# Optimization experiments

Measured on AMD Instinct MI355X. Metric: run time of the kernel, lower is better.

The kernel has to match this reference:

```python
import jax, jax.numpy as jnp
import numpy as np

D_MODEL, N_HEADS, D_K, D_V = 1024, 16, 64, 64
B, S = 4, 1024
LN_EPS = 1e-5


def setup_inputs() -> dict:
    key = jax.random.key(0)
    ks = jax.random.split(key, 12)
    s = 0.02
    # causal mask: True = masked (mimics masked_fill_ semantics)
    mask = jnp.triu(jnp.ones((S, S), dtype=bool), k=1)
    mask = jnp.broadcast_to(mask, (B, S, S))
    return {
        "Q": jax.random.normal(ks[0], (B, S, D_MODEL), jnp.float32),
        "K": jax.random.normal(ks[1], (B, S, D_MODEL), jnp.float32),
        "V": jax.random.normal(ks[2], (B, S, D_MODEL), jnp.float32),
        "mask": mask,
        # Linear params stored as [in, out] (equivalent to torch weight.T)
        "Wq": jax.random.normal(ks[3], (D_MODEL, N_HEADS * D_K), jnp.float32) * s,
        "bq": jnp.zeros((N_HEADS * D_K,), jnp.float32),
        "Wk": jax.random.normal(ks[4], (D_MODEL, N_HEADS * D_K), jnp.float32) * s,
        "bk": jnp.zeros((N_HEADS * D_K,), jnp.float32),
        "Wv": jax.random.normal(ks[5], (D_MODEL, N_HEADS * D_V), jnp.float32) * s,
        "bv": jnp.zeros((N_HEADS * D_V,), jnp.float32),
        "Wo": jax.random.normal(ks[6], (N_HEADS * D_V, D_MODEL), jnp.float32) * s,
        "bo": jnp.zeros((D_MODEL,), jnp.float32),
        "gamma": jnp.ones((D_MODEL,), jnp.float32),
        "beta": jnp.zeros((D_MODEL,), jnp.float32),
    }


def reference(Q, K, V, mask, Wq, bq, Wk, bk, Wv, bv, Wo, bo, gamma, beta):
    b, sq, _ = Q.shape
    sk = K.shape[1]
    residual = Q
    # projections -> [b, h, s, d]
    q = (Q @ Wq + bq).reshape(b, sq, N_HEADS, D_K).transpose(0, 2, 1, 3)
    k = (K @ Wk + bk).reshape(b, sk, N_HEADS, D_K).transpose(0, 2, 1, 3)
    v = (V @ Wv + bv).reshape(b, sk, N_HEADS, D_V).transpose(0, 2, 1, 3)
    scale = 1.0 / np.sqrt(D_K).astype(np.float32)
    scores = jnp.einsum("bhqd,bhkd->bhqk", q, k) * scale  # [b,h,sq,sk]
    scores = jnp.where(mask[:, None, :, :], jnp.float32(-1e9), scores)
    attn = jax.nn.softmax(scores, axis=-1)
    out = jnp.einsum("bhqk,bhkd->bhqd", attn, v)
    out = out.transpose(0, 2, 1, 3).reshape(b, sq, N_HEADS * D_V)
    out = out @ Wo + bo
    # LayerNorm(out + residual)
    x = out + residual
    mu = jnp.mean(x, axis=-1, keepdims=True)
    var = jnp.mean(jnp.square(x - mu), axis=-1, keepdims=True)
    y = (x - mu) * jax.lax.rsqrt(var + LN_EPS) * gamma + beta
    return (y, attn)
```

## Files before the change

kernel.cpp:

```cpp
#include <hip/hip_runtime.h>
#include <stdint.h>

#define B_ 4
#define S_ 1024
#define H_ 16
#define D_ 64
#define DM 1024
#define M_ (B_*S_)

using bf16x8 = __attribute__((ext_vector_type(8))) short;
using f32x4  = __attribute__((ext_vector_type(4))) float;

__device__ inline unsigned short f2bf(float f) {
  unsigned u = __float_as_uint(f);
  u += 0x7fff + ((u >> 16) & 1);
  return (unsigned short)(u >> 16);
}
__device__ inline float bf2f(unsigned short s) {
  return __uint_as_float(((unsigned)s) << 16);
}

__global__ __launch_bounds__(256) void cvt_f32_bf16(const float* __restrict__ src,
                                                    unsigned short* __restrict__ dst, int n4) {
  int i = blockIdx.x * 256 + threadIdx.x;
  if (i < n4) {
    float4 v = ((const float4*)src)[i];
    ushort4 o;
    o.x = f2bf(v.x); o.y = f2bf(v.y); o.z = f2bf(v.z); o.w = f2bf(v.w);
    ((ushort4*)dst)[i] = o;
  }
}

__global__ __launch_bounds__(256) void transpose_cvt(const float* w0, const float* w1,
                                                     const float* w2, const float* w3,
                                                     unsigned short* o0, unsigned short* o1,
                                                     unsigned short* o2, unsigned short* o3) {
  const float* src; unsigned short* dst;
  switch (blockIdx.z) {
    case 0: src = w0; dst = o0; break;
    case 1: src = w1; dst = o1; break;
    case 2: src = w2; dst = o2; break;
    default: src = w3; dst = o3; break;
  }
  __shared__ float t[32][33];
  int tx = threadIdx.x, ty = threadIdx.y;
  int x = blockIdx.x * 32 + tx;
  for (int i = 0; i < 4; i++) {
    int y = blockIdx.y * 32 + ty + i * 8;
    t[ty + i * 8][tx] = src[y * DM + x];
  }
  __syncthreads();
  int xo = blockIdx.y * 32 + tx;
  for (int i = 0; i < 4; i++) {
    int yo = blockIdx.x * 32 + ty + i * 8;
    dst[yo * DM + xo] = f2bf(t[tx][ty + i * 8]);
  }
}

__global__ __launch_bounds__(256) void gemm_nt(const unsigned short* __restrict__ X,
                                               const unsigned short* __restrict__ WT,
                                               const float* __restrict__ bias,
                                               void* __restrict__ out, int mode) {
  __shared__ unsigned short Al[64][32];
  __shared__ unsigned short Bl[64][32];
  int t = threadIdx.x;
  int lane = t & 63, w = t >> 6;
  int quad = lane >> 4, l16 = lane & 15;
  int wm = w & 1, wn = w >> 1;
  int m0 = blockIdx.y * 64, n0 = blockIdx.x * 64;
  f32x4 acc[2][2] = {};
  int arow = t >> 2, acol = (t & 3) * 8;
  for (int k0 = 0; k0 < DM; k0 += 32) {
    *(uint4*)&Al[arow][acol] = *(const uint4*)&X [((size_t)(m0 + arow)) * DM + k0 + acol];
    *(uint4*)&Bl[arow][acol] = *(const uint4*)&WT[((size_t)(n0 + arow)) * DM + k0 + acol];
    __syncthreads();
    bf16x8 af[2], bf[2];
    for (int ms = 0; ms < 2; ms++) af[ms] = *(const bf16x8*)&Al[wm * 32 + ms * 16 + l16][quad * 8];
    for (int ns = 0; ns < 2; ns++) bf[ns] = *(const bf16x8*)&Bl[wn * 32 + ns * 16 + l16][quad * 8];
    for (int ms = 0; ms < 2; ms++)
      for (int ns = 0; ns < 2; ns++)
        acc[ms][ns] = __builtin_amdgcn_mfma_f32_16x16x32_bf16(af[ms], bf[ns], acc[ms][ns], 0, 0, 0);
    __syncthreads();
  }
  for (int ms = 0; ms < 2; ms++)
    for (int ns = 0; ns < 2; ns++)
      for (int r = 0; r < 4; r++) {
        int gm = m0 + wm * 32 + ms * 16 + quad * 4 + r;
        int gn = n0 + wn * 32 + ns * 16 + l16;
        float v = acc[ms][ns][r] + bias[gn];
        if (mode == 2) {
          ((float*)out)[(size_t)gm * DM + gn] = v;
        } else {
          int b = gm >> 10, s = gm & 1023, h = gn >> 6, d = gn & 63;
          if (mode == 0)
            ((unsigned short*)out)[(((size_t)(b * H_ + h)) * S_ + s) * D_ + d] = f2bf(v);
          else
            ((unsigned short*)out)[(((size_t)(b * H_ + h)) * D_ + d) * S_ + s] = f2bf(v);
        }
      }
}

__global__ __launch_bounds__(256) void attn_kernel(const unsigned short* __restrict__ qp,
                                                   const unsigned short* __restrict__ kp,
                                                   const unsigned short* __restrict__ vT,
                                                   float* __restrict__ attn_out,
                                                   unsigned short* __restrict__ ctx) {
  __shared__ unsigned short Srow[16][1032];
  __shared__ unsigned short Qt[16][64];
  __shared__ float red[16][16];
  __shared__ float rmax[16];
  __shared__ float rinv[16];
  int t = threadIdx.x;
  int lane = t & 63, w = t >> 6, quad = lane >> 4, l16 = lane & 15;
  int bx = blockIdx.x;
  int qt = bx & 63, h = (bx >> 6) & 15, b = bx >> 10;
  int bh = b * H_ + h;
  const int L = (qt + 1) * 16;

  {
    int r = t >> 4, d = (t & 15) * 4;
    const unsigned short* src = qp + (((size_t)bh * S_) + qt * 16 + r) * D_ + d;
    ushort4 v = *(const ushort4*)src;
    Qt[r][d + 0] = f2bf(bf2f(v.x) * 0.125f);
    Qt[r][d + 1] = f2bf(bf2f(v.y) * 0.125f);
    Qt[r][d + 2] = f2bf(bf2f(v.z) * 0.125f);
    Qt[r][d + 3] = f2bf(bf2f(v.w) * 0.125f);
  }
  __syncthreads();

  for (int ct = w; ct <= qt; ct += 4) {
    f32x4 acc = {};
    for (int d0 = 0; d0 < 64; d0 += 32) {
      bf16x8 af = *(const bf16x8*)&Qt[l16][d0 + quad * 8];
      bf16x8 bfr = *(const bf16x8*)&kp[(((size_t)bh * S_) + ct * 16 + l16) * D_ + d0 + quad * 8];
      acc = __builtin_amdgcn_mfma_f32_16x16x32_bf16(af, bfr, acc, 0, 0, 0);
    }
    for (int r = 0; r < 4; r++) {
      int row = quad * 4 + r;
      int gq = qt * 16 + row, gk = ct * 16 + l16;
      Srow[row][ct * 16 + l16] = f2bf((gk <= gq) ? acc[r] : -1e30f);
    }
  }
  __syncthreads();

  int row = t & 15, chunk = t >> 4;
  float m = -1e30f;
  for (int c = chunk; c < L; c += 16) m = fmaxf(m, bf2f(Srow[row][c]));
  red[row][chunk] = m;
  __syncthreads();
  if (t < 16) {
    float mm = -1e30f;
    for (int j = 0; j < 16; j++) mm = fmaxf(mm, red[t][j]);
    rmax[t] = mm;
  }
  __syncthreads();
  float mr = rmax[row], sum = 0.f;
  for (int c = chunk; c < L; c += 16) {
    float e = __expf(bf2f(Srow[row][c]) - mr);
    Srow[row][c] = f2bf(e);
    sum += e;
  }
  red[row][chunk] = sum;
  __syncthreads();
  if (t < 16) {
    float l = 0.f;
    for (int j = 0; j < 16; j++) l += red[t][j];
    rinv[t] = 1.0f / l;
  }
  __syncthreads();

  float* outbase = attn_out + (((size_t)bh) * S_ + qt * 16) * S_;
  for (int idx = t; idx < 16 * 1024; idx += 256) {
    int rr = idx >> 10, cc = idx & 1023;
    float v = (cc < L) ? bf2f(Srow[rr][cc]) * rinv[rr] : 0.f;
    outbase[(size_t)rr * S_ + cc] = v;
  }
  if (L & 31) {
    Srow[t & 15][L + (t >> 4)] = 0;
  }
  __syncthreads();

  int K32 = (L + 31) >> 5;
  f32x4 oacc = {};
  int n = w * 16 + l16;
  for (int kk = 0; kk < K32; kk++) {
    int k0 = kk * 32;
    bf16x8 af = *(const bf16x8*)&Srow[l16][k0 + quad * 8];
    bf16x8 bfr = *(const bf16x8*)&vT[(((size_t)bh) * D_ + n) * S_ + k0 + quad * 8];
    oacc = __builtin_amdgcn_mfma_f32_16x16x32_bf16(af, bfr, oacc, 0, 0, 0);
  }
  for (int r = 0; r < 4; r++) {
    int rr = quad * 4 + r;
    ctx[(((size_t)b * S_) + qt * 16 + rr) * DM + h * D_ + n] = f2bf(oacc[r] * rinv[rr]);
  }
}

__global__ __launch_bounds__(256) void ln_kernel(const float* __restrict__ y0,
                                                 const float* __restrict__ resid,
                                                 const float* __restrict__ gamma,
                                                 const float* __restrict__ beta,
                                                 float* __restrict__ out) {
  int row = blockIdx.x, t = threadIdx.x;
  float x[4]; float s = 0.f, s2 = 0.f;
  for (int i = 0; i < 4; i++) {
    int c = t + i * 256;
    float v = y0[(size_t)row * DM + c] + resid[(size_t)row * DM + c];
    x[i] = v; s += v; s2 += v * v;
  }
  for (int off = 32; off; off >>= 1) {
    s  += __shfl_down(s,  off, 64);
    s2 += __shfl_down(s2, off, 64);
  }
  __shared__ float ws1[4], ws2[4];
  __shared__ float mu_s, rv_s;
  int wv = t >> 6, lane = t & 63;
  if (lane == 0) { ws1[wv] = s; ws2[wv] = s2; }
  __syncthreads();
  if (t == 0) {
    float ts = ws1[0] + ws1[1] + ws1[2] + ws1[3];
    float ts2 = ws2[0] + ws2[1] + ws2[2] + ws2[3];
    float mu = ts / DM;
    float var = ts2 / DM - mu * mu;
    mu_s = mu; rv_s = rsqrtf(var + 1e-5f);
  }
  __syncthreads();
  float mu = mu_s, rv = rv_s;
  for (int i = 0; i < 4; i++) {
    int c = t + i * 256;
    out[(size_t)row * DM + c] = (x[i] - mu) * rv * gamma[c] + beta[c];
  }
}

extern "C" void kernel_launch(void* const* d_in, const int* in_sizes, int n_in,
                              void* d_out, int out_size, void* d_ws, size_t ws_size,
                              hipStream_t stream) {
  const float* Qf = (const float*)d_in[0];
  const float* Kf = (const float*)d_in[1];
  const float* Vf = (const float*)d_in[2];
  const float* Wq = (const float*)d_in[4];
  const float* bq = (const float*)d_in[5];
  const float* Wk = (const float*)d_in[6];
  const float* bk = (const float*)d_in[7];
  const float* Wv = (const float*)d_in[8];
  const float* bv = (const float*)d_in[9];
  const float* Wo = (const float*)d_in[10];
  const float* bo = (const float*)d_in[11];
  const float* gamma = (const float*)d_in[12];
  const float* beta  = (const float*)d_in[13];

  char* ws = (char*)d_ws;
  unsigned short* Qb  = (unsigned short*)(ws + 0);
  unsigned short* ctx = (unsigned short*)(ws + 0);
  unsigned short* Kb  = (unsigned short*)(ws + 8388608);
  unsigned short* Vb  = (unsigned short*)(ws + 16777216);
  float*          y0  = (float*)(ws + 8388608);
  unsigned short* WqT = (unsigned short*)(ws + 25165824);
  unsigned short* WkT = (unsigned short*)(ws + 27262976);
  unsigned short* WvT = (unsigned short*)(ws + 29360128);
  unsigned short* WoT = (unsigned short*)(ws + 31457280);
  unsigned short* qp  = (unsigned short*)(ws + 33554432);
  unsigned short* kp  = (unsigned short*)(ws + 41943040);
  unsigned short* vTp = (unsigned short*)(ws + 50331648);

  float* y_out    = (float*)d_out;
  float* attn_out = (float*)d_out + (size_t)M_ * DM;

  int n4 = M_ * DM / 4;
  cvt_f32_bf16<<<dim3(n4 / 256), dim3(256), 0, stream>>>(Qf, Qb, n4);
  cvt_f32_bf16<<<dim3(n4 / 256), dim3(256), 0, stream>>>(Kf, Kb, n4);
  cvt_f32_bf16<<<dim3(n4 / 256), dim3(256), 0, stream>>>(Vf, Vb, n4);
  transpose_cvt<<<dim3(32, 32, 4), dim3(32, 8), 0, stream>>>(Wq, Wk, Wv, Wo, WqT, WkT, WvT, WoT);

  dim3 ggrid(DM / 64, M_ / 64);
  gemm_nt<<<ggrid, 256, 0, stream>>>(Qb, WqT, bq, qp, 0);
  gemm_nt<<<ggrid, 256, 0, stream>>>(Kb, WkT, bk, kp, 0);
  gemm_nt<<<ggrid, 256, 0, stream>>>(Vb, WvT, bv, vTp, 1);

  attn_kernel<<<dim3(B_ * H_ * (S_ / 16)), 256, 0, stream>>>(qp, kp, vTp, attn_out, ctx);

  gemm_nt<<<ggrid, 256, 0, stream>>>(ctx, WoT, bo, y0, 2);
  ln_kernel<<<dim3(M_), 256, 0, stream>>>(y0, Qf, gamma, beta, y_out);
}
```

Baseline: 557.0 us.

## Widen GEMM tiles with direct LDS loads, fold Q scale into weights, vectorize softmax

The GEMM tile grows from 64x64 to 64x128 and global-to-LDS staging now uses global_load_lds, which reduces per-block load traffic and register staging. The 1/sqrt(d) query scale is folded into the transposed Wq and its bias, so the attention kernel reads Q straight from global memory without a scaled LDS copy. The softmax passes and the attention-probability writes are vectorized to 8-element LDS reads and float4 global stores. The wider tile halves the GEMM grid, and the new row mapping changes the LDS access pattern.

```diff
diff --git a/kernel.cpp b/kernel.cpp
--- a/kernel.cpp
+++ b/kernel.cpp
@@ -8,20 +8,29 @@
 #define DM 1024
 #define M_ (B_*S_)
 
+typedef unsigned short ushort_t;
+typedef unsigned int u32;
 using bf16x8 = __attribute__((ext_vector_type(8))) short;
 using f32x4  = __attribute__((ext_vector_type(4))) float;
 
-__device__ inline unsigned short f2bf(float f) {
+__device__ inline ushort_t f2bf(float f) {
   unsigned u = __float_as_uint(f);
   u += 0x7fff + ((u >> 16) & 1);
-  return (unsigned short)(u >> 16);
-}
-__device__ inline float bf2f(unsigned short s) {
+  return (ushort_t)(u >> 16);
+}
+__device__ inline float bf2f(ushort_t s) {
   return __uint_as_float(((unsigned)s) << 16);
 }
 
+__device__ __forceinline__ void gl2lds16(const void* g, void* l) {
+  __builtin_amdgcn_global_load_lds(
+      (const __attribute__((address_space(1))) u32*)g,
+      (__attribute__((address_space(3))) u32*)l,
+      16, 0, 0);
+}
+
 __global__ __launch_bounds__(256) void cvt_f32_bf16(const float* __restrict__ src,
-                                                    unsigned short* __restrict__ dst, int n4) {
+                                                    ushort_t* __restrict__ dst, int n4) {
   int i = blockIdx.x * 256 + threadIdx.x;
   if (i < n4) {
     float4 v = ((const float4*)src)[i];
@@ -33,15 +42,16 @@
 
 __global__ __launch_bounds__(256) void transpose_cvt(const float* w0, const float* w1,
                                                      const float* w2, const float* w3,
-                                                     unsigned short* o0, unsigned short* o1,
-                                                     unsigned short* o2, unsigned short* o3) {
-  const float* src; unsigned short* dst;
+                                                     ushort_t* o0, ushort_t* o1,
+                                                     ushort_t* o2, ushort_t* o3) {
+  const float* src; ushort_t* dst;
   switch (blockIdx.z) {
     case 0: src = w0; dst = o0; break;
     case 1: src = w1; dst = o1; break;
     case 2: src = w2; dst = o2; break;
     default: src = w3; dst = o3; break;
   }
+  float scl = (blockIdx.z == 0) ? 0.125f : 1.0f;
   __shared__ float t[32][33];
   int tx = threadIdx.x, ty = threadIdx.y;
   int x = blockIdx.x * 32 + tx;
@@ -53,60 +63,67 @@
   int xo = blockIdx.y * 32 + tx;
   for (int i = 0; i < 4; i++) {
     int yo = blockIdx.x * 32 + ty + i * 8;
-    dst[yo * DM + xo] = f2bf(t[tx][ty + i * 8]);
-  }
-}
-
-__global__ __launch_bounds__(256) void gemm_nt(const unsigned short* __restrict__ X,
-                                               const unsigned short* __restrict__ WT,
-                                               const float* __restrict__ bias,
-                                               void* __restrict__ out, int mode) {
-  __shared__ unsigned short Al[64][32];
-  __shared__ unsigned short Bl[64][32];
+    dst[yo * DM + xo] = f2bf(t[tx][ty + i * 8] * scl);
+  }
+}
+
+#define BM 64
+#define BN 128
+__global__ __launch_bounds__(256, 4) void gemm_nt(const ushort_t* __restrict__ X,
+                                                  const ushort_t* __restrict__ WT,
+                                                  const float* __restrict__ bias, float bscale,
+                                                  void* __restrict__ out, int mode) {
+  __shared__ ushort_t Al[BM][32];
+  __shared__ ushort_t Bl[BN][32];
   int t = threadIdx.x;
-  int lane = t & 63, w = t >> 6;
-  int quad = lane >> 4, l16 = lane & 15;
+  int lane = t & 63, w = t >> 6, quad = lane >> 4, l16 = lane & 15;
   int wm = w & 1, wn = w >> 1;
-  int m0 = blockIdx.y * 64, n0 = blockIdx.x * 64;
-  f32x4 acc[2][2] = {};
-  int arow = t >> 2, acol = (t & 3) * 8;
+  int m0 = blockIdx.y * BM, n0 = blockIdx.x * BN;
+  f32x4 acc[2][4] = {};
+  int r4 = t >> 2, c8 = (t & 3) * 8;
+  const ushort_t* ga  = X  + (size_t)(m0 + r4) * DM + c8;
+  const ushort_t* gb0 = WT + (size_t)(n0 + r4) * DM + c8;
+  const ushort_t* gb1 = WT + (size_t)(n0 + 64 + r4) * DM + c8;
+  ushort_t* la  = &Al[r4][c8];
+  ushort_t* lb0 = &Bl[r4][c8];
+  ushort_t* lb1 = &Bl[64 + r4][c8];
   for (int k0 = 0; k0 < DM; k0 += 32) {
-    *(uint4*)&Al[arow][acol] = *(const uint4*)&X [((size_t)(m0 + arow)) * DM + k0 + acol];
-    *(uint4*)&Bl[arow][acol] = *(const uint4*)&WT[((size_t)(n0 + arow)) * DM + k0 + acol];
+    gl2lds16(ga  + k0, la);
+    gl2lds16(gb0 + k0, lb0);
+    gl2lds16(gb1 + k0, lb1);
     __syncthreads();
-    bf16x8 af[2], bf[2];
-    for (int ms = 0; ms < 2; ms++) af[ms] = *(const bf16x8*)&Al[wm * 32 + ms * 16 + l16][quad * 8];
-    for (int ns = 0; ns < 2; ns++) bf[ns] = *(const bf16x8*)&Bl[wn * 32 + ns * 16 + l16][quad * 8];
+    bf16x8 af[2], bfv[4];
+    for (int ms = 0; ms < 2; ms++) af[ms]  = *(const bf16x8*)&Al[wm * 32 + ms * 16 + l16][quad * 8];
+    for (int ns = 0; ns < 4; ns++) bfv[ns] = *(const bf16x8*)&Bl[wn * 64 + ns * 16 + l16][quad * 8];
     for (int ms = 0; ms < 2; ms++)
-      for (int ns = 0; ns < 2; ns++)
-        acc[ms][ns] = __builtin_amdgcn_mfma_f32_16x16x32_bf16(af[ms], bf[ns], acc[ms][ns], 0, 0, 0);
+      for (int ns = 0; ns < 4; ns++)
+        acc[ms][ns] = __builtin_amdgcn_mfma_f32_16x16x32_bf16(af[ms], bfv[ns], acc[ms][ns], 0, 0, 0);
     __syncthreads();
   }
   for (int ms = 0; ms < 2; ms++)
-    for (int ns = 0; ns < 2; ns++)
+    for (int ns = 0; ns < 4; ns++)
       for (int r = 0; r < 4; r++) {
         int gm = m0 + wm * 32 + ms * 16 + quad * 4 + r;
-        int gn = n0 + wn * 32 + ns * 16 + l16;
-        float v = acc[ms][ns][r] + bias[gn];
+        int gn = n0 + wn * 64 + ns * 16 + l16;
+        float v = acc[ms][ns][r] + bias[gn] * bscale;
         if (mode == 2) {
           ((float*)out)[(size_t)gm * DM + gn] = v;
         } else {
           int b = gm >> 10, s = gm & 1023, h = gn >> 6, d = gn & 63;
           if (mode == 0)
-            ((unsigned short*)out)[(((size_t)(b * H_ + h)) * S_ + s) * D_ + d] = f2bf(v);
+            ((ushort_t*)out)[(((size_t)(b * H_ + h)) * S_ + s) * D_ + d] = f2bf(v);
           else
-            ((unsigned short*)out)[(((size_t)(b * H_ + h)) * D_ + d) * S_ + s] = f2bf(v);
+            ((ushort_t*)out)[(((size_t)(b * H_ + h)) * D_ + d) * S_ + s] = f2bf(v);
         }
       }
 }
 
-__global__ __launch_bounds__(256) void attn_kernel(const unsigned short* __restrict__ qp,
-                                                   const unsigned short* __restrict__ kp,
-                                                   const unsigned short* __restrict__ vT,
+__global__ __launch_bounds__(256) void attn_kernel(const ushort_t* __restrict__ qp,
+                                                   const ushort_t* __restrict__ kp,
+                                                   const ushort_t* __restrict__ vT,
                                                    float* __restrict__ attn_out,
-                                                   unsigned short* __restrict__ ctx) {
-  __shared__ unsigned short Srow[16][1032];
-  __shared__ unsigned short Qt[16][64];
+                                                   ushort_t* __restrict__ ctx) {
+  __shared__ ushort_t Srow[16][1032];
   __shared__ float red[16][16];
   __shared__ float rmax[16];
   __shared__ float rinv[16];
@@ -117,21 +134,11 @@
   int bh = b * H_ + h;
   const int L = (qt + 1) * 16;
 
-  {
-    int r = t >> 4, d = (t & 15) * 4;
-    const unsigned short* src = qp + (((size_t)bh * S_) + qt * 16 + r) * D_ + d;
-    ushort4 v = *(const ushort4*)src;
-    Qt[r][d + 0] = f2bf(bf2f(v.x) * 0.125f);
-    Qt[r][d + 1] = f2bf(bf2f(v.y) * 0.125f);
-    Qt[r][d + 2] = f2bf(bf2f(v.z) * 0.125f);
-    Qt[r][d + 3] = f2bf(bf2f(v.w) * 0.125f);
-  }
-  __syncthreads();
-
+  const ushort_t* qbase = qp + (((size_t)bh * S_) + qt * 16 + l16) * D_;
   for (int ct = w; ct <= qt; ct += 4) {
     f32x4 acc = {};
     for (int d0 = 0; d0 < 64; d0 += 32) {
-      bf16x8 af = *(const bf16x8*)&Qt[l16][d0 + quad * 8];
+      bf16x8 af  = *(const bf16x8*)&qbase[d0 + quad * 8];
       bf16x8 bfr = *(const bf16x8*)&kp[(((size_t)bh * S_) + ct * 16 + l16) * D_ + d0 + quad * 8];
       acc = __builtin_amdgcn_mfma_f32_16x16x32_bf16(af, bfr, acc, 0, 0, 0);
     }
@@ -143,10 +150,16 @@
   }
   __syncthreads();
 
-  int row = t & 15, chunk = t >> 4;
+  int row = t >> 4, sub = t & 15;
   float m = -1e30f;
-  for (int c = chunk; c < L; c += 16) m = fmaxf(m, bf2f(Srow[row][c]));
-  red[row][chunk] = m;
+  for (int i = 0; i < 8; i++) {
+    int c = (sub + 16 * i) * 8;
+    if (c < L) {
+      bf16x8 v = *(const bf16x8*)&Srow[row][c];
+      for (int j = 0; j < 8; j++) m = fmaxf(m, bf2f((ushort_t)v[j]));
+    }
+  }
+  red[row][sub] = m;
   __syncthreads();
   if (t < 16) {
     float mm = -1e30f;
@@ -154,13 +167,22 @@
     rmax[t] = mm;
   }
   __syncthreads();
+
   float mr = rmax[row], sum = 0.f;
-  for (int c = chunk; c < L; c += 16) {
-    float e = __expf(bf2f(Srow[row][c]) - mr);
-    Srow[row][c] = f2bf(e);
-    sum += e;
-  }
-  red[row][chunk] = sum;
+  for (int i = 0; i < 8; i++) {
+    int c = (sub + 16 * i) * 8;
+    if (c < L) {
+      bf16x8 v = *(const bf16x8*)&Srow[row][c];
+      bf16x8 e;
+      for (int j = 0; j < 8; j++) {
+        float ev = __expf(bf2f((ushort_t)v[j]) - mr);
+        e[j] = (short)f2bf(ev);
+        sum += ev;
+      }
+      *(bf16x8*)&Srow[row][c] = e;
+    }
+  }
+  red[row][sub] = sum;
   __syncthreads();
   if (t < 16) {
     float l = 0.f;
@@ -170,10 +192,19 @@
   __syncthreads();
 
   float* outbase = attn_out + (((size_t)bh) * S_ + qt * 16) * S_;
-  for (int idx = t; idx < 16 * 1024; idx += 256) {
-    int rr = idx >> 10, cc = idx & 1023;
-    float v = (cc < L) ? bf2f(Srow[rr][cc]) * rinv[rr] : 0.f;
-    outbase[(size_t)rr * S_ + cc] = v;
+  float ri = rinv[row];
+  for (int i = 0; i < 8; i++) {
+    int c = (sub + 16 * i) * 8;
+    float4 o0 = {0.f, 0.f, 0.f, 0.f}, o1 = {0.f, 0.f, 0.f, 0.f};
+    if (c < L) {
+      bf16x8 v = *(const bf16x8*)&Srow[row][c];
+      o0.x = bf2f((ushort_t)v[0]) * ri; o0.y = bf2f((ushort_t)v[1]) * ri;
+      o0.z = bf2f((ushort_t)v[2]) * ri; o0.w = bf2f((ushort_t)v[3]) * ri;
+      o1.x = bf2f((ushort_t)v[4]) * ri; o1.y = bf2f((ushort_t)v[5]) * ri;
+      o1.z = bf2f((ushort_t)v[6]) * ri; o1.w = bf2f((ushort_t)v[7]) * ri;
+    }
+    *(float4*)&outbase[(size_t)row * S_ + c]     = o0;
+    *(float4*)&outbase[(size_t)row * S_ + c + 4] = o1;
   }
   if (L & 31) {
     Srow[t & 15][L + (t >> 4)] = 0;
@@ -185,7 +216,7 @@
   int n = w * 16 + l16;
   for (int kk = 0; kk < K32; kk++) {
     int k0 = kk * 32;
-    bf16x8 af = *(const bf16x8*)&Srow[l16][k0 + quad * 8];
+    bf16x8 af  = *(const bf16x8*)&Srow[l16][k0 + quad * 8];
     bf16x8 bfr = *(const bf16x8*)&vT[(((size_t)bh) * D_ + n) * S_ + k0 + quad * 8];
     oacc = __builtin_amdgcn_mfma_f32_16x16x32_bf16(af, bfr, oacc, 0, 0, 0);
   }
@@ -271,13 +302,13 @@
   cvt_f32_bf16<<<dim3(n4 / 256), dim3(256), 0, stream>>>(Vf, Vb, n4);
   transpose_cvt<<<dim3(32, 32, 4), dim3(32, 8), 0, stream>>>(Wq, Wk, Wv, Wo, WqT, WkT, WvT, WoT);
 
-  dim3 ggrid(DM / 64, M_ / 64);
-  gemm_nt<<<ggrid, 256, 0, stream>>>(Qb, WqT, bq, qp, 0);
-  gemm_nt<<<ggrid, 256, 0, stream>>>(Kb, WkT, bk, kp, 0);
-  gemm_nt<<<ggrid, 256, 0, stream>>>(Vb, WvT, bv, vTp, 1);
+  dim3 ggrid(DM / BN, M_ / BM);
+  gemm_nt<<<ggrid, 256, 0, stream>>>(Qb, WqT, bq, 0.125f, qp, 0);
+  gemm_nt<<<ggrid, 256, 0, stream>>>(Kb, WkT, bk, 1.0f, kp, 0);
+  gemm_nt<<<ggrid, 256, 0, stream>>>(Vb, WvT, bv, 1.0f, vTp, 1);
 
   attn_kernel<<<dim3(B_ * H_ * (S_ / 16)), 256, 0, stream>>>(qp, kp, vTp, attn_out, ctx);
 
-  gemm_nt<<<ggrid, 256, 0, stream>>>(ctx, WoT, bo, y0, 2);
+  gemm_nt<<<ggrid, 256, 0, stream>>>(ctx, WoT, bo, 1.0f, y0, 2);
   ln_kernel<<<dim3(M_), 256, 0, stream>>>(y0, Qf, gamma, beta, y_out);
 }
```

New measurement: 542.5 us. -2.6%, faster.
